# Performance work log

Hardware: AMD Instinct MI355X
Metric: run time of the kernel (lower is better)

Reference implementation:

```python
import math
import jax, jax.numpy as jnp
import numpy as np

B, DZ, DX, U = 262144, 8, 16, 64


def setup_inputs() -> dict:
    key = jax.random.key(0)
    ks = jax.random.split(key, 12)
    s = lambda k, shape, scale=1.0: (jax.random.normal(k, shape, dtype=jnp.float32) * scale)
    return {
        "h": s(ks[0], (B, U), 0.1),
        "c": s(ks[1], (B, U), 0.1),
        "z_prev": s(ks[2], (B, DZ)),
        "x_t": s(ks[3], (B, DX)),
        "W_kernel": s(ks[4], (DZ, 4 * U), 1.0 / math.sqrt(DZ)),
        "W_recurrent": s(ks[5], (U, 4 * U), 1.0 / math.sqrt(U)),
        "b_lstm": jnp.zeros((4 * U,), jnp.float32),
        "W_mu": s(ks[6], (U, DZ), 1.0 / math.sqrt(U)),
        "b_mu": jnp.zeros((DZ,), jnp.float32),
        "W_log_sigma": s(ks[7], (U, DZ), 1.0 / math.sqrt(U)),
        "b_log_sigma": -jnp.ones((DZ,), jnp.float32),  # Constant(-1.0) bias init
        "C": jnp.eye(DX, DZ, dtype=jnp.float32) + s(ks[8], (DX, DZ), 0.05),
        "b_emission": jnp.zeros((DX,), jnp.float32),
        "log_R_diag": jnp.zeros((DX,), jnp.float32),
    }


def reference(h, c, z_prev, x_t, W_kernel, W_recurrent, b_lstm,
              W_mu, b_mu, W_log_sigma, b_log_sigma, C, b_emission, log_R_diag):
    dz, dx = C.shape[1], C.shape[0]
    # --- Keras LSTMCell step (gate order: i, f, g, o) ---
    z = z_prev @ W_kernel + h @ W_recurrent + b_lstm  # [B, 4U]
    i, f, g, o = jnp.split(z, 4, axis=-1)
    c_new = jax.nn.sigmoid(f) * c + jax.nn.sigmoid(i) * jnp.tanh(g)
    h_new = jax.nn.sigmoid(o) * jnp.tanh(c_new)
    # --- transition params ---
    mu = h_new @ W_mu + b_mu                                        # [B, dz]
    log_sigma = jnp.clip(h_new @ W_log_sigma + b_log_sigma, -5.0, 3.0)
    sigma = jnp.exp(log_sigma)
    Sigma_diag = sigma ** 2                                          # [B, dz]
    R_diag = jnp.exp(log_R_diag)                                     # [dx]
    # --- alpha: log N(x_t; C mu + b, R + C diag(Sigma) C^T) ---
    pred_mean = mu @ C.T + b_emission                                # [B, dx]
    C_scaled = C[None, :, :] * jnp.sqrt(Sigma_diag)[:, None, :]      # [B, dx, dz]
    base = jnp.eye(dx, dtype=C.dtype) * R_diag + jnp.eye(dx, dtype=C.dtype) * 1e-6
    marg_cov = base[None] + jnp.einsum('bik,bjk->bij', C_scaled, C_scaled)  # [B, dx, dx]
    _, log_det = jnp.linalg.slogdet(marg_cov)
    marg_inv = jnp.linalg.inv(marg_cov)
    diff_x = x_t - pred_mean
    mahal = jnp.einsum('bi,bij,bj->b', diff_x, marg_inv, diff_x)
    alpha = -0.5 * (mahal + log_det + dx * math.log(2.0 * math.pi))  # [B]
    # --- gamma: posterior over z_t ---
    Sigma_inv_diag = 1.0 / (Sigma_diag + 1e-8)                       # [B, dz]
    R_inv_diag = 1.0 / (R_diag + 1e-8)                               # [dx]
    CtRinvC = (C * R_inv_diag[:, None]).T @ C                        # [dz, dz]
    V_inv = (jnp.eye(dz, dtype=C.dtype) * Sigma_inv_diag[:, None, :]
             + CtRinvC[None] + jnp.eye(dz, dtype=C.dtype) * 1e-6)    # [B, dz, dz]
    V = jnp.linalg.inv(V_inv)
    info = Sigma_inv_diag * mu + ((x_t - b_emission) * R_inv_diag) @ C  # [B, dz]
    gamma_mu = jnp.einsum('bij,bj->bi', V, info)                     # [B, dz]
    return alpha, gamma_mu, V, h_new, c_new
```

## Files before the change

kernel.cpp:

```cpp
#include <hip/hip_runtime.h>
#include <math.h>

#define BATCH 262144

#define WA_OFF  0
#define G6_OFF  18944
#define G8_OFF  19008
#define R6_OFF  19072
#define R8_OFF  19088
#define SLR_OFF 19104

typedef __attribute__((ext_vector_type(8))) short bf16x8;
typedef __attribute__((ext_vector_type(4))) float f32x4;

__device__ __forceinline__ float rcp1(float x) {
    float r = __builtin_amdgcn_rcpf(x);
    return r * (2.0f - x * r);
}
__device__ __forceinline__ float sigm(float x) {
    float e = __expf(-fabsf(x));
    float s = __builtin_amdgcn_rcpf(1.0f + e);
    return (x >= 0.0f) ? s : e * s;
}
__device__ __forceinline__ float tanh_f(float x) {
    float e = __expf(-2.0f * fabsf(x));
    float t = (1.0f - e) * __builtin_amdgcn_rcpf(1.0f + e);
    return copysignf(t, x);
}
__device__ __forceinline__ unsigned rne_bf16(float x) {
    unsigned u = __float_as_uint(x);
    return (u + 0x7fffu + ((u >> 16) & 1u)) >> 16;
}
__device__ __forceinline__ unsigned pack2(float lo, float hi) {
    return rne_bf16(lo) | (rne_bf16(hi) << 16);
}

__global__ void prep_kernel(const float* __restrict__ Wk,
                            const float* __restrict__ Wr,
                            const float* __restrict__ Cm,
                            const float* __restrict__ logR,
                            float* __restrict__ ws) {
    int b = blockIdx.x;
    int t = threadIdx.x;
    if (b < 12) {
        unsigned* wa = (unsigned*)(ws + WA_OFF);
        int F  = b * 256 + t;
        int fr = F >> 6, l = F & 63;
        int m  = fr / 3, ks = fr % 3;
        int c  = m * 16 + (l & 15);
        int k0 = ks * 32 + (l >> 4) * 8;
        int src = (c & 3) * 64 + (c >> 2);
        float v[8];
#pragma unroll
        for (int j = 0; j < 8; ++j) {
            int k = k0 + j;
            v[j] = (k < 8) ? Wk[k * 256 + src] : (k < 72 ? Wr[(k - 8) * 256 + src] : 0.0f);
        }
        wa[F * 4 + 0] = pack2(v[0], v[1]);
        wa[F * 4 + 1] = pack2(v[2], v[3]);
        wa[F * 4 + 2] = pack2(v[4], v[5]);
        wa[F * 4 + 3] = pack2(v[6], v[7]);
        return;
    }
    if (t < 64) {
        int k = t >> 3, l = t & 7;
        float g6 = 0.0f, g8 = 0.0f;
        for (int i = 0; i < 16; ++i) {
            float R  = expf(logR[i]);
            float cc = Cm[i * 8 + k] * Cm[i * 8 + l];
            g6 += cc / (R + 1e-6f);
            g8 += cc / (R + 1e-8f);
        }
        ws[G6_OFF + t] = g6;
        ws[G8_OFF + t] = g8;
    } else if (t < 80) {
        int i = t - 64;
        float R = expf(logR[i]);
        ws[R6_OFF + i] = 1.0f / (R + 1e-6f);
        ws[R8_OFF + i] = 1.0f / (R + 1e-8f);
    } else if (t == 80) {
        float s = 0.0f;
        for (int i = 0; i < 16; ++i) s += logf(expf(logR[i]) + 1e-6f);
        ws[SLR_OFF] = s;
    }
}

__global__ __launch_bounds__(256)
void lstm_kernel(const float* __restrict__ h_in,
                 const float* __restrict__ c_in,
                 const float* __restrict__ z_prev,
                 const float* __restrict__ b_lstm,
                 const float* __restrict__ W_mu,
                 const float* __restrict__ b_mu,
                 const float* __restrict__ W_ls,
                 const float* __restrict__ b_ls,
                 const float* __restrict__ ws,
                 float* __restrict__ out) {
    __shared__ __align__(16) float r1[64 * 72];
    __shared__ __align__(16) float r2[64 * 68];

    const int t   = threadIdx.x;
    const int l   = t & 63;
    const int wvu = __builtin_amdgcn_readfirstlane(t >> 6);
    const int lhi = l >> 4, llo = l & 15;
    const size_t E0 = (size_t)blockIdx.x * 64;

#pragma unroll
    for (int i = 0; i < 4; ++i) {
        int g = i * 1024 + t * 4;
        int e = g >> 6, u = g & 63;
        float4 hv = *(const float4*)(h_in + E0 * 64 + g);
        *(float4*)(r1 + e * 72 + 8 + u) = hv;
    }
    if (t < 128) {
        int g = t * 4;
        int e = g >> 3, p = g & 7;
        float4 zv = *(const float4*)(z_prev + E0 * 8 + g);
        *(float4*)(r1 + e * 72 + p) = zv;
    }
    __syncthreads();

    unsigned* fr = (unsigned*)r2;
#pragma unroll
    for (int i = 0; i < 3; ++i) {
        int c = i * 256 + t;
        if (c < 576) {
            int e = c / 9, k0 = (c % 9) * 8;
            float4 va = *(const float4*)(r1 + c * 8);
            float4 vb = *(const float4*)(r1 + c * 8 + 4);
            uint4 pk;
            pk.x = pack2(va.x, va.y);
            pk.y = pack2(va.z, va.w);
            pk.z = pack2(vb.x, vb.y);
            pk.w = pack2(vb.z, vb.w);
            int n = e >> 4, lo = e & 15, ks = k0 >> 5, hi = (k0 & 31) >> 3;
            int F = (n * 3 + ks) * 64 + hi * 16 + lo;
            *(uint4*)(fr + F * 4) = pk;
        }
    }
    if (t < 192) {
        int n = t / 48, r = t % 48;
        int hi = r / 16 + 1, lo = r & 15;
        int F = (n * 3 + 2) * 64 + hi * 16 + lo;
        *(uint4*)(fr + F * 4) = make_uint4(0, 0, 0, 0);
    }
    __syncthreads();

    float4 cp0 = *(const float4*)(c_in + E0 * 64 + 0 * 1024 + t * 4);
    float4 cp1 = *(const float4*)(c_in + E0 * 64 + 1 * 1024 + t * 4);
    float4 cp2 = *(const float4*)(c_in + E0 * 64 + 2 * 1024 + t * 4);
    float4 cp3 = *(const float4*)(c_in + E0 * 64 + 3 * 1024 + t * 4);

    f32x4 acc[4][4];
#pragma unroll
    for (int mm = 0; mm < 4; ++mm)
#pragma unroll
        for (int n = 0; n < 4; ++n) acc[mm][n] = (f32x4){0.f, 0.f, 0.f, 0.f};

    const unsigned* WA = (const unsigned*)(ws + WA_OFF);
#pragma unroll
    for (int ks = 0; ks < 3; ++ks) {
        bf16x8 bfr[4], afr[4];
#pragma unroll
        for (int n = 0; n < 4; ++n)
            bfr[n] = *(const bf16x8*)(fr + ((n * 3 + ks) * 64 + l) * 4);
#pragma unroll
        for (int mm = 0; mm < 4; ++mm)
            afr[mm] = *(const bf16x8*)(WA + (((4 * wvu + mm) * 3 + ks) * 64 + l) * 4);
#pragma unroll
        for (int mm = 0; mm < 4; ++mm)
#pragma unroll
            for (int n = 0; n < 4; ++n)
                acc[mm][n] = __builtin_amdgcn_mfma_f32_16x16x32_bf16(
                    afr[mm], bfr[n], acc[mm][n], 0, 0, 0);
    }

    float* cbuf = r1;
    {
        int g0 = t * 4;
        *(float4*)(cbuf + ((g0 >> 6)) * 68 + (g0 & 63)) = cp0;
        int g1 = 1024 + t * 4;
        *(float4*)(cbuf + ((g1 >> 6)) * 68 + (g1 & 63)) = cp1;
        int g2 = 2048 + t * 4;
        *(float4*)(cbuf + ((g2 >> 6)) * 68 + (g2 & 63)) = cp2;
        int g3 = 3072 + t * 4;
        *(float4*)(cbuf + ((g3 >> 6)) * 68 + (g3 & 63)) = cp3;
    }
    __syncthreads();

    float* hbuf = r2;
#pragma unroll
    for (int mm = 0; mm < 4; ++mm) {
        int u = 16 * wvu + 4 * mm + lhi;
        float bi = b_lstm[u], bf_ = b_lstm[64 + u], bg = b_lstm[128 + u], bo = b_lstm[192 + u];
#pragma unroll
        for (int n = 0; n < 4; ++n) {
            int e = n * 16 + llo;
            float zi = acc[mm][n][0] + bi;
            float zf = acc[mm][n][1] + bf_;
            float zg = acc[mm][n][2] + bg;
            float zo = acc[mm][n][3] + bo;
            float cold = cbuf[e * 68 + u];
            float cn = sigm(zf) * cold + sigm(zi) * tanh_f(zg);
            float hn = sigm(zo) * tanh_f(cn);
            cbuf[e * 68 + u] = cn;
            hbuf[u * 68 + e] = hn;
        }
    }
    __syncthreads();

    float* outH = out + (size_t)BATCH * 73  + E0 * 64;
    float* outC = out + (size_t)BATCH * 137 + E0 * 64;
#pragma unroll
    for (int i = 0; i < 4; ++i) {
        int g = i * 1024 + t * 4;
        int e = g >> 6, u = g & 63;
        *(float4*)(outC + g) = *(const float4*)(cbuf + e * 68 + u);
        float4 hv = make_float4(hbuf[(u + 0) * 68 + e], hbuf[(u + 1) * 68 + e],
                                hbuf[(u + 2) * 68 + e], hbuf[(u + 3) * 68 + e]);
        *(float4*)(outH + g) = hv;
    }

    {
        const float* Wsel = (wvu < 2) ? W_mu : W_ls;
        const float* bsel = (wvu < 2) ? b_mu : b_ls;
        const int d0 = (wvu & 1) * 4;
        float m0 = bsel[d0 + 0], m1 = bsel[d0 + 1], m2 = bsel[d0 + 2], m3 = bsel[d0 + 3];
#pragma unroll
        for (int u = 0; u < 64; ++u) {
            float hv = hbuf[u * 68 + l];
            m0 = fmaf(hv, Wsel[u * 8 + d0 + 0], m0);
            m1 = fmaf(hv, Wsel[u * 8 + d0 + 1], m1);
            m2 = fmaf(hv, Wsel[u * 8 + d0 + 2], m2);
            m3 = fmaf(hv, Wsel[u * 8 + d0 + 3], m3);
        }
        float* slot = out + (size_t)BATCH * 9 + (E0 + l) * 64 + wvu * 4;
        *(float4*)slot = make_float4(m0, m1, m2, m3);
    }
}

__global__ __launch_bounds__(256)
void tail_kernel(const float* __restrict__ x_in,
                 const float* __restrict__ Cm,
                 const float* __restrict__ b_em,
                 const float* __restrict__ ws,
                 float* __restrict__ out) {
    __shared__ float vbuf[64 * 65];

    const int t    = threadIdx.x;
    const int lane = t & 63;
    const int wv   = t >> 6;
    const int blk  = blockIdx.x;
    const size_t e = (size_t)blk * 256 + t;

    const float* G6 = ws + G6_OFF;
    const float* G8 = ws + G8_OFF;
    const float* r6 = ws + R6_OFF;
    const float* r8 = ws + R8_OFF;
    const float  slr = ws[SLR_OFF];

    const float* tmp = out + (size_t)BATCH * 9 + e * 64;
    float4 q0 = *(const float4*)(tmp + 0);
    float4 q1 = *(const float4*)(tmp + 4);
    float4 q2 = *(const float4*)(tmp + 8);
    float4 q3 = *(const float4*)(tmp + 12);
    float mu[8]  = {q0.x, q0.y, q0.z, q0.w, q1.x, q1.y, q1.z, q1.w};
    float lsg[8] = {q2.x, q2.y, q2.z, q2.w, q3.x, q3.y, q3.z, q3.w};

    float sig[8], Sinv[8];
#pragma unroll
    for (int d = 0; d < 8; ++d) {
        float l = fminf(fmaxf(lsg[d], -5.0f), 3.0f);
        float s = __expf(l);
        sig[d]  = s;
        Sinv[d] = rcp1(s * s + 1e-8f);
    }

    float xv[16];
    {
        const float4* x4 = (const float4*)(x_in + e * 16);
#pragma unroll
        for (int q = 0; q < 4; ++q) {
            float4 v = x4[q];
            xv[4 * q + 0] = v.x; xv[4 * q + 1] = v.y;
            xv[4 * q + 2] = v.z; xv[4 * q + 3] = v.w;
        }
    }

    float t6[8], t8[8];
#pragma unroll
    for (int k = 0; k < 8; ++k) { t6[k] = 0.0f; t8[k] = 0.0f; }
    float qdr = 0.0f;
#pragma unroll
    for (int i = 0; i < 16; ++i) {
        float pm = b_em[i];
#pragma unroll
        for (int d = 0; d < 8; ++d) pm = fmaf(mu[d], Cm[i * 8 + d], pm);
        float df = xv[i] - pm;
        float xe = xv[i] - b_em[i];
        float a6 = df * r6[i];
        float a8 = xe * r8[i];
        qdr = fmaf(df, a6, qdr);
#pragma unroll
        for (int k = 0; k < 8; ++k) {
            t6[k] = fmaf(a6, Cm[i * 8 + k], t6[k]);
            t8[k] = fmaf(a8, Cm[i * 8 + k], t8[k]);
        }
    }

    float M[8][8];
#pragma unroll
    for (int k = 0; k < 8; ++k)
#pragma unroll
        for (int l = 0; l <= k; ++l)
            M[k][l] = ((k == l) ? 1.0f : 0.0f) + sig[k] * sig[l] * G6[k * 8 + l];

    float ldia[8];
    float logdetM = 0.0f;
#pragma unroll
    for (int k = 0; k < 8; ++k) {
        float d = M[k][k];
#pragma unroll
        for (int j = 0; j < k; ++j) d = fmaf(-M[k][j], M[k][j], d);
        float l = sqrtf(d);
        logdetM += __logf(d);
        float li = rcp1(l);
        M[k][k] = l; ldia[k] = li;
#pragma unroll
        for (int i = k + 1; i < 8; ++i) {
            float s = M[i][k];
#pragma unroll
            for (int j = 0; j < k; ++j) s = fmaf(-M[i][j], M[k][j], s);
            M[i][k] = s * li;
        }
    }
    float w[8];
    float ssq = 0.0f;
#pragma unroll
    for (int k = 0; k < 8; ++k) {
        float s = sig[k] * t6[k];
#pragma unroll
        for (int j = 0; j < k; ++j) s = fmaf(-M[k][j], w[j], s);
        w[k] = s * ldia[k];
        ssq  = fmaf(w[k], w[k], ssq);
    }
    float mahal  = qdr - ssq;
    float alpha  = -0.5f * (mahal + slr + logdetM + 29.40603306254952f);

    float Vi[8][8];
#pragma unroll
    for (int k = 0; k < 8; ++k)
#pragma unroll
        for (int l = 0; l <= k; ++l)
            Vi[k][l] = G8[k * 8 + l] + ((k == l) ? (Sinv[k] + 1e-6f) : 0.0f);

    float vdia[8];
#pragma unroll
    for (int k = 0; k < 8; ++k) {
        float d = Vi[k][k];
#pragma unroll
        for (int j = 0; j < k; ++j) d = fmaf(-Vi[k][j], Vi[k][j], d);
        float l = sqrtf(d);
        float li = rcp1(l);
        Vi[k][k] = l; vdia[k] = li;
#pragma unroll
        for (int i = k + 1; i < 8; ++i) {
            float s = Vi[i][k];
#pragma unroll
            for (int j = 0; j < k; ++j) s = fmaf(-Vi[i][j], Vi[k][j], s);
            Vi[i][k] = s * li;
        }
    }
#pragma unroll
    for (int k = 0; k < 8; ++k) {
        M[k][k] = vdia[k];
#pragma unroll
        for (int i = k + 1; i < 8; ++i) {
            float s = 0.0f;
#pragma unroll
            for (int j = k; j < i; ++j) s = fmaf(Vi[i][j], M[j][k], s);
            M[i][k] = -s * vdia[i];
        }
    }
    float info[8];
#pragma unroll
    for (int k = 0; k < 8; ++k) info[k] = fmaf(Sinv[k], mu[k], t8[k]);

#pragma unroll 1
    for (int ch = 0; ch < 4; ++ch) {
        if (wv == ch) {
            float gam[8];
#pragma unroll
            for (int a = 0; a < 8; ++a) gam[a] = 0.0f;
#pragma unroll
            for (int a = 0; a < 8; ++a) {
#pragma unroll
                for (int b = 0; b < 8; ++b) {
                    int m0 = (a > b) ? a : b;
                    float s = 0.0f;
#pragma unroll
                    for (int i = 0; i < 8; ++i)
                        if (i >= m0) s = fmaf(M[i][a], M[i][b], s);
                    vbuf[(a * 8 + b) * 65 + lane] = s;
                    gam[a] = fmaf(s, info[b], gam[a]);
                }
            }
            out[e] = alpha;
            float4* outG = (float4*)(out + (size_t)BATCH + e * 8);
            outG[0] = make_float4(gam[0], gam[1], gam[2], gam[3]);
            outG[1] = make_float4(gam[4], gam[5], gam[6], gam[7]);
        }
        __syncthreads();
        {
            float* outV = out + (size_t)BATCH * 9 + ((size_t)blk * 256 + (size_t)ch * 64) * 64;
#pragma unroll
            for (int i = 0; i < 4; ++i) {
                int g = i * 1024 + t * 4;
                int ee = g >> 6, j = g & 63;
                float4 v = make_float4(vbuf[(j + 0) * 65 + ee], vbuf[(j + 1) * 65 + ee],
                                       vbuf[(j + 2) * 65 + ee], vbuf[(j + 3) * 65 + ee]);
                *(float4*)(outV + g) = v;
            }
        }
        __syncthreads();
    }
}

extern "C" void kernel_launch(void* const* d_in, const int* in_sizes, int n_in,
                              void* d_out, int out_size, void* d_ws, size_t ws_size,
                              hipStream_t stream) {
    const float* h    = (const float*)d_in[0];
    const float* c    = (const float*)d_in[1];
    const float* zp   = (const float*)d_in[2];
    const float* xt   = (const float*)d_in[3];
    const float* Wk   = (const float*)d_in[4];
    const float* Wr   = (const float*)d_in[5];
    const float* bl   = (const float*)d_in[6];
    const float* Wmu  = (const float*)d_in[7];
    const float* bmu  = (const float*)d_in[8];
    const float* Wls  = (const float*)d_in[9];
    const float* bls  = (const float*)d_in[10];
    const float* Cm   = (const float*)d_in[11];
    const float* bem  = (const float*)d_in[12];
    const float* logR = (const float*)d_in[13];
    float* ws  = (float*)d_ws;
    float* out = (float*)d_out;

    hipLaunchKernelGGL(prep_kernel, dim3(13), dim3(256), 0, stream, Wk, Wr, Cm, logR, ws);
    hipLaunchKernelGGL(lstm_kernel, dim3(BATCH / 64), dim3(256), 0, stream,
                       h, c, zp, bl, Wmu, bmu, Wls, bls, ws, out);
    hipLaunchKernelGGL(tail_kernel, dim3(BATCH / 256), dim3(256), 0, stream,
                       xt, Cm, bem, ws, out);
}
```

Before: 111.8 us.

## Fuse LSTM and tail kernels, passing mu/log_sigma through shared memory

Merges the LSTM kernel and the Kalman tail kernel into one kernel in which each block handles 256 batch rows as four 64-row LSTM tiles. The mu/log_sigma values go into a shared-memory buffer instead of being written to global memory and read back by a second launch. This removes the global round-trip of the intermediate values and one kernel launch. In exchange the grid has a quarter as many blocks, the LSTM tiles run one after another inside each block, and more LDS is used per block, which can lower occupancy and latency hiding.

```diff
diff --git a/kernel.cpp b/kernel.cpp
--- a/kernel.cpp
+++ b/kernel.cpp
@@ -86,192 +86,192 @@
 }
 
 __global__ __launch_bounds__(256)
-void lstm_kernel(const float* __restrict__ h_in,
-                 const float* __restrict__ c_in,
-                 const float* __restrict__ z_prev,
-                 const float* __restrict__ b_lstm,
-                 const float* __restrict__ W_mu,
-                 const float* __restrict__ b_mu,
-                 const float* __restrict__ W_ls,
-                 const float* __restrict__ b_ls,
-                 const float* __restrict__ ws,
-                 float* __restrict__ out) {
+void fused_kernel(const float* __restrict__ h_in,
+                  const float* __restrict__ c_in,
+                  const float* __restrict__ z_prev,
+                  const float* __restrict__ x_in,
+                  const float* __restrict__ b_lstm,
+                  const float* __restrict__ W_mu,
+                  const float* __restrict__ b_mu,
+                  const float* __restrict__ W_ls,
+                  const float* __restrict__ b_ls,
+                  const float* __restrict__ Cm,
+                  const float* __restrict__ b_em,
+                  const float* __restrict__ ws,
+                  float* __restrict__ out) {
     __shared__ __align__(16) float r1[64 * 72];
     __shared__ __align__(16) float r2[64 * 68];
+    __shared__ float muls[16 * 257];
 
     const int t   = threadIdx.x;
     const int l   = t & 63;
     const int wvu = __builtin_amdgcn_readfirstlane(t >> 6);
     const int lhi = l >> 4, llo = l & 15;
-    const size_t E0 = (size_t)blockIdx.x * 64;
-
-#pragma unroll
-    for (int i = 0; i < 4; ++i) {
-        int g = i * 1024 + t * 4;
-        int e = g >> 6, u = g & 63;
-        float4 hv = *(const float4*)(h_in + E0 * 64 + g);
-        *(float4*)(r1 + e * 72 + 8 + u) = hv;
-    }
-    if (t < 128) {
-        int g = t * 4;
-        int e = g >> 3, p = g & 7;
-        float4 zv = *(const float4*)(z_prev + E0 * 8 + g);
-        *(float4*)(r1 + e * 72 + p) = zv;
+    const size_t B0 = (size_t)blockIdx.x * 256;
+    const unsigned* WA = (const unsigned*)(ws + WA_OFF);
+
+#pragma unroll 1
+    for (int tile = 0; tile < 4; ++tile) {
+        const size_t E0 = B0 + (size_t)tile * 64;
+        __syncthreads();
+
+#pragma unroll
+        for (int i = 0; i < 4; ++i) {
+            int g = i * 1024 + t * 4;
+            int e = g >> 6, u = g & 63;
+            float4 hv = *(const float4*)(h_in + E0 * 64 + g);
+            *(float4*)(r1 + e * 72 + 8 + u) = hv;
+        }
+        if (t < 128) {
+            int g = t * 4;
+            int e = g >> 3, p = g & 7;
+            float4 zv = *(const float4*)(z_prev + E0 * 8 + g);
+            *(float4*)(r1 + e * 72 + p) = zv;
+        }
+        __syncthreads();
+
+        unsigned* fr = (unsigned*)r2;
+#pragma unroll
+        for (int i = 0; i < 3; ++i) {
+            int c = i * 256 + t;
+            if (c < 576) {
+                int e = c / 9, k0 = (c % 9) * 8;
+                float4 va = *(const float4*)(r1 + c * 8);
+                float4 vb = *(const float4*)(r1 + c * 8 + 4);
+                uint4 pk;
+                pk.x = pack2(va.x, va.y);
+                pk.y = pack2(va.z, va.w);
+                pk.z = pack2(vb.x, vb.y);
+                pk.w = pack2(vb.z, vb.w);
+                int n = e >> 4, lo = e & 15, ks = k0 >> 5, hi = (k0 & 31) >> 3;
+                int F = (n * 3 + ks) * 64 + hi * 16 + lo;
+                *(uint4*)(fr + F * 4) = pk;
+            }
+        }
+        if (t < 192) {
+            int n = t / 48, r = t % 48;
+            int hi = r / 16 + 1, lo = r & 15;
+            int F = (n * 3 + 2) * 64 + hi * 16 + lo;
+            *(uint4*)(fr + F * 4) = make_uint4(0, 0, 0, 0);
+        }
+        __syncthreads();
+
+        float4 cp0 = *(const float4*)(c_in + E0 * 64 + 0 * 1024 + t * 4);
+        float4 cp1 = *(const float4*)(c_in + E0 * 64 + 1 * 1024 + t * 4);
+        float4 cp2 = *(const float4*)(c_in + E0 * 64 + 2 * 1024 + t * 4);
+        float4 cp3 = *(const float4*)(c_in + E0 * 64 + 3 * 1024 + t * 4);
+
+        f32x4 acc[4][4];
+#pragma unroll
+        for (int mm = 0; mm < 4; ++mm)
+#pragma unroll
+            for (int n = 0; n < 4; ++n) acc[mm][n] = (f32x4){0.f, 0.f, 0.f, 0.f};
+#pragma unroll
+        for (int ks = 0; ks < 3; ++ks) {
+            bf16x8 bfr[4], afr[4];
+#pragma unroll
+            for (int n = 0; n < 4; ++n)
+                bfr[n] = *(const bf16x8*)(fr + ((n * 3 + ks) * 64 + l) * 4);
+#pragma unroll
+            for (int mm = 0; mm < 4; ++mm)
+                afr[mm] = *(const bf16x8*)(WA + (((4 * wvu + mm) * 3 + ks) * 64 + l) * 4);
+#pragma unroll
+            for (int mm = 0; mm < 4; ++mm)
+#pragma unroll
+                for (int n = 0; n < 4; ++n)
+                    acc[mm][n] = __builtin_amdgcn_mfma_f32_16x16x32_bf16(
+                        afr[mm], bfr[n], acc[mm][n], 0, 0, 0);
+        }
+
+        float* cbuf = r1;
+        {
+            int g0 = t * 4;
+            *(float4*)(cbuf + ((g0 >> 6)) * 68 + (g0 & 63)) = cp0;
+            int g1 = 1024 + t * 4;
+            *(float4*)(cbuf + ((g1 >> 6)) * 68 + (g1 & 63)) = cp1;
+            int g2 = 2048 + t * 4;
+            *(float4*)(cbuf + ((g2 >> 6)) * 68 + (g2 & 63)) = cp2;
+            int g3 = 3072 + t * 4;
+            *(float4*)(cbuf + ((g3 >> 6)) * 68 + (g3 & 63)) = cp3;
+        }
+        __syncthreads();
+
+        float* hbuf = r2;
+#pragma unroll
+        for (int mm = 0; mm < 4; ++mm) {
+            int u = 16 * wvu + 4 * mm + lhi;
+            float bi = b_lstm[u], bf_ = b_lstm[64 + u], bg = b_lstm[128 + u], bo = b_lstm[192 + u];
+#pragma unroll
+            for (int n = 0; n < 4; ++n) {
+                int e = n * 16 + llo;
+                float zi = acc[mm][n][0] + bi;
+                float zf = acc[mm][n][1] + bf_;
+                float zg = acc[mm][n][2] + bg;
+                float zo = acc[mm][n][3] + bo;
+                float cold = cbuf[e * 68 + u];
+                float cn = sigm(zf) * cold + sigm(zi) * tanh_f(zg);
+                float hn = sigm(zo) * tanh_f(cn);
+                cbuf[e * 68 + u] = cn;
+                hbuf[u * 68 + e] = hn;
+            }
+        }
+        __syncthreads();
+
+        float* outH = out + (size_t)BATCH * 73  + E0 * 64;
+        float* outC = out + (size_t)BATCH * 137 + E0 * 64;
+#pragma unroll
+        for (int i = 0; i < 4; ++i) {
+            int g = i * 1024 + t * 4;
+            int e = g >> 6, u = g & 63;
+            *(float4*)(outC + g) = *(const float4*)(cbuf + e * 68 + u);
+            float4 hv = make_float4(hbuf[(u + 0) * 68 + e], hbuf[(u + 1) * 68 + e],
+                                    hbuf[(u + 2) * 68 + e], hbuf[(u + 3) * 68 + e]);
+            *(float4*)(outH + g) = hv;
+        }
+
+        {
+            const float* Wsel = (wvu < 2) ? W_mu : W_ls;
+            const float* bsel = (wvu < 2) ? b_mu : b_ls;
+            const int d0 = (wvu & 1) * 4;
+            const int row0 = (wvu < 2) ? d0 : 8 + d0;
+            float m0 = bsel[d0 + 0], m1 = bsel[d0 + 1], m2 = bsel[d0 + 2], m3 = bsel[d0 + 3];
+#pragma unroll
+            for (int u = 0; u < 64; ++u) {
+                float hv = hbuf[u * 68 + l];
+                m0 = fmaf(hv, Wsel[u * 8 + d0 + 0], m0);
+                m1 = fmaf(hv, Wsel[u * 8 + d0 + 1], m1);
+                m2 = fmaf(hv, Wsel[u * 8 + d0 + 2], m2);
+                m3 = fmaf(hv, Wsel[u * 8 + d0 + 3], m3);
+            }
+            int col = tile * 64 + l;
+            muls[(row0 + 0) * 257 + col] = m0;
+            muls[(row0 + 1) * 257 + col] = m1;
+            muls[(row0 + 2) * 257 + col] = m2;
+            muls[(row0 + 3) * 257 + col] = m3;
+        }
     }
     __syncthreads();
-
-    unsigned* fr = (unsigned*)r2;
-#pragma unroll
-    for (int i = 0; i < 3; ++i) {
-        int c = i * 256 + t;
-        if (c < 576) {
-            int e = c / 9, k0 = (c % 9) * 8;
-            float4 va = *(const float4*)(r1 + c * 8);
-            float4 vb = *(const float4*)(r1 + c * 8 + 4);
-            uint4 pk;
-            pk.x = pack2(va.x, va.y);
-            pk.y = pack2(va.z, va.w);
-            pk.z = pack2(vb.x, vb.y);
-            pk.w = pack2(vb.z, vb.w);
-            int n = e >> 4, lo = e & 15, ks = k0 >> 5, hi = (k0 & 31) >> 3;
-            int F = (n * 3 + ks) * 64 + hi * 16 + lo;
-            *(uint4*)(fr + F * 4) = pk;
-        }
-    }
-    if (t < 192) {
-        int n = t / 48, r = t % 48;
-        int hi = r / 16 + 1, lo = r & 15;
-        int F = (n * 3 + 2) * 64 + hi * 16 + lo;
-        *(uint4*)(fr + F * 4) = make_uint4(0, 0, 0, 0);
-    }
-    __syncthreads();
-
-    float4 cp0 = *(const float4*)(c_in + E0 * 64 + 0 * 1024 + t * 4);
-    float4 cp1 = *(const float4*)(c_in + E0 * 64 + 1 * 1024 + t * 4);
-    float4 cp2 = *(const float4*)(c_in + E0 * 64 + 2 * 1024 + t * 4);
-    float4 cp3 = *(const float4*)(c_in + E0 * 64 + 3 * 1024 + t * 4);
-
-    f32x4 acc[4][4];
-#pragma unroll
-    for (int mm = 0; mm < 4; ++mm)
-#pragma unroll
-        for (int n = 0; n < 4; ++n) acc[mm][n] = (f32x4){0.f, 0.f, 0.f, 0.f};
-
-    const unsigned* WA = (const unsigned*)(ws + WA_OFF);
-#pragma unroll
-    for (int ks = 0; ks < 3; ++ks) {
-        bf16x8 bfr[4], afr[4];
-#pragma unroll
-        for (int n = 0; n < 4; ++n)
-            bfr[n] = *(const bf16x8*)(fr + ((n * 3 + ks) * 64 + l) * 4);
-#pragma unroll
-        for (int mm = 0; mm < 4; ++mm)
-            afr[mm] = *(const bf16x8*)(WA + (((4 * wvu + mm) * 3 + ks) * 64 + l) * 4);
-#pragma unroll
-        for (int mm = 0; mm < 4; ++mm)
-#pragma unroll
-            for (int n = 0; n < 4; ++n)
-                acc[mm][n] = __builtin_amdgcn_mfma_f32_16x16x32_bf16(
-                    afr[mm], bfr[n], acc[mm][n], 0, 0, 0);
-    }
-
-    float* cbuf = r1;
-    {
-        int g0 = t * 4;
-        *(float4*)(cbuf + ((g0 >> 6)) * 68 + (g0 & 63)) = cp0;
-        int g1 = 1024 + t * 4;
-        *(float4*)(cbuf + ((g1 >> 6)) * 68 + (g1 & 63)) = cp1;
-        int g2 = 2048 + t * 4;
-        *(float4*)(cbuf + ((g2 >> 6)) * 68 + (g2 & 63)) = cp2;
-        int g3 = 3072 + t * 4;
-        *(float4*)(cbuf + ((g3 >> 6)) * 68 + (g3 & 63)) = cp3;
-    }
-    __syncthreads();
-
-    float* hbuf = r2;
-#pragma unroll
-    for (int mm = 0; mm < 4; ++mm) {
-        int u = 16 * wvu + 4 * mm + lhi;
-        float bi = b_lstm[u], bf_ = b_lstm[64 + u], bg = b_lstm[128 + u], bo = b_lstm[192 + u];
-#pragma unroll
-        for (int n = 0; n < 4; ++n) {
-            int e = n * 16 + llo;
-            float zi = acc[mm][n][0] + bi;
-            float zf = acc[mm][n][1] + bf_;
-            float zg = acc[mm][n][2] + bg;
-            float zo = acc[mm][n][3] + bo;
-            float cold = cbuf[e * 68 + u];
-            float cn = sigm(zf) * cold + sigm(zi) * tanh_f(zg);
-            float hn = sigm(zo) * tanh_f(cn);
-            cbuf[e * 68 + u] = cn;
-            hbuf[u * 68 + e] = hn;
-        }
-    }
-    __syncthreads();
-
-    float* outH = out + (size_t)BATCH * 73  + E0 * 64;
-    float* outC = out + (size_t)BATCH * 137 + E0 * 64;
-#pragma unroll
-    for (int i = 0; i < 4; ++i) {
-        int g = i * 1024 + t * 4;
-        int e = g >> 6, u = g & 63;
-        *(float4*)(outC + g) = *(const float4*)(cbuf + e * 68 + u);
-        float4 hv = make_float4(hbuf[(u + 0) * 68 + e], hbuf[(u + 1) * 68 + e],
-                                hbuf[(u + 2) * 68 + e], hbuf[(u + 3) * 68 + e]);
-        *(float4*)(outH + g) = hv;
-    }
-
-    {
-        const float* Wsel = (wvu < 2) ? W_mu : W_ls;
-        const float* bsel = (wvu < 2) ? b_mu : b_ls;
-        const int d0 = (wvu & 1) * 4;
-        float m0 = bsel[d0 + 0], m1 = bsel[d0 + 1], m2 = bsel[d0 + 2], m3 = bsel[d0 + 3];
-#pragma unroll
-        for (int u = 0; u < 64; ++u) {
-            float hv = hbuf[u * 68 + l];
-            m0 = fmaf(hv, Wsel[u * 8 + d0 + 0], m0);
-            m1 = fmaf(hv, Wsel[u * 8 + d0 + 1], m1);
-            m2 = fmaf(hv, Wsel[u * 8 + d0 + 2], m2);
-            m3 = fmaf(hv, Wsel[u * 8 + d0 + 3], m3);
-        }
-        float* slot = out + (size_t)BATCH * 9 + (E0 + l) * 64 + wvu * 4;
-        *(float4*)slot = make_float4(m0, m1, m2, m3);
-    }
-}
-
-__global__ __launch_bounds__(256)
-void tail_kernel(const float* __restrict__ x_in,
-                 const float* __restrict__ Cm,
-                 const float* __restrict__ b_em,
-                 const float* __restrict__ ws,
-                 float* __restrict__ out) {
-    __shared__ float vbuf[64 * 65];
-
-    const int t    = threadIdx.x;
-    const int lane = t & 63;
-    const int wv   = t >> 6;
-    const int blk  = blockIdx.x;
-    const size_t e = (size_t)blk * 256 + t;
 
     const float* G6 = ws + G6_OFF;
     const float* G8 = ws + G8_OFF;
     const float* r6 = ws + R6_OFF;
     const float* r8 = ws + R8_OFF;
     const float  slr = ws[SLR_OFF];
-
-    const float* tmp = out + (size_t)BATCH * 9 + e * 64;
-    float4 q0 = *(const float4*)(tmp + 0);
-    float4 q1 = *(const float4*)(tmp + 4);
-    float4 q2 = *(const float4*)(tmp + 8);
-    float4 q3 = *(const float4*)(tmp + 12);
-    float mu[8]  = {q0.x, q0.y, q0.z, q0.w, q1.x, q1.y, q1.z, q1.w};
-    float lsg[8] = {q2.x, q2.y, q2.z, q2.w, q3.x, q3.y, q3.z, q3.w};
+    const size_t e = B0 + t;
+    const int wv = t >> 6;
+
+    float mu[8], lsg[8];
+#pragma unroll
+    for (int d = 0; d < 8; ++d) {
+        mu[d]  = muls[d * 257 + t];
+        lsg[d] = muls[(8 + d) * 257 + t];
+    }
 
     float sig[8], Sinv[8];
 #pragma unroll
     for (int d = 0; d < 8; ++d) {
-        float l = fminf(fmaxf(lsg[d], -5.0f), 3.0f);
-        float s = __expf(l);
+        float lv = fminf(fmaxf(lsg[d], -5.0f), 3.0f);
+        float s = __expf(lv);
         sig[d]  = s;
         Sinv[d] = rcp1(s * s + 1e-8f);
     }
@@ -312,8 +312,8 @@
 #pragma unroll
     for (int k = 0; k < 8; ++k)
 #pragma unroll
-        for (int l = 0; l <= k; ++l)
-            M[k][l] = ((k == l) ? 1.0f : 0.0f) + sig[k] * sig[l] * G6[k * 8 + l];
+        for (int lq = 0; lq <= k; ++lq)
+            M[k][lq] = ((k == lq) ? 1.0f : 0.0f) + sig[k] * sig[lq] * G6[k * 8 + lq];
 
     float ldia[8];
     float logdetM = 0.0f;
@@ -322,10 +322,10 @@
         float d = M[k][k];
 #pragma unroll
         for (int j = 0; j < k; ++j) d = fmaf(-M[k][j], M[k][j], d);
-        float l = sqrtf(d);
+        float lv = sqrtf(d);
         logdetM += __logf(d);
-        float li = rcp1(l);
-        M[k][k] = l; ldia[k] = li;
+        float li = rcp1(lv);
+        M[k][k] = lv; ldia[k] = li;
 #pragma unroll
         for (int i = k + 1; i < 8; ++i) {
             float s = M[i][k];
@@ -344,15 +344,15 @@
         w[k] = s * ldia[k];
         ssq  = fmaf(w[k], w[k], ssq);
     }
-    float mahal  = qdr - ssq;
-    float alpha  = -0.5f * (mahal + slr + logdetM + 29.40603306254952f);
+    float mahal = qdr - ssq;
+    float alpha = -0.5f * (mahal + slr + logdetM + 29.40603306254952f);
 
     float Vi[8][8];
 #pragma unroll
     for (int k = 0; k < 8; ++k)
 #pragma unroll
-        for (int l = 0; l <= k; ++l)
-            Vi[k][l] = G8[k * 8 + l] + ((k == l) ? (Sinv[k] + 1e-6f) : 0.0f);
+        for (int lq = 0; lq <= k; ++lq)
+            Vi[k][lq] = G8[k * 8 + lq] + ((k == lq) ? (Sinv[k] + 1e-6f) : 0.0f);
 
     float vdia[8];
 #pragma unroll
@@ -360,9 +360,9 @@
         float d = Vi[k][k];
 #pragma unroll
         for (int j = 0; j < k; ++j) d = fmaf(-Vi[k][j], Vi[k][j], d);
-        float l = sqrtf(d);
-        float li = rcp1(l);
-        Vi[k][k] = l; vdia[k] = li;
+        float lv = sqrtf(d);
+        float li = rcp1(lv);
+        Vi[k][k] = lv; vdia[k] = li;
 #pragma unroll
         for (int i = k + 1; i < 8; ++i) {
             float s = Vi[i][k];
@@ -386,6 +386,7 @@
 #pragma unroll
     for (int k = 0; k < 8; ++k) info[k] = fmaf(Sinv[k], mu[k], t8[k]);
 
+    float* vbuf = r1;
 #pragma unroll 1
     for (int ch = 0; ch < 4; ++ch) {
         if (wv == ch) {
@@ -401,7 +402,7 @@
 #pragma unroll
                     for (int i = 0; i < 8; ++i)
                         if (i >= m0) s = fmaf(M[i][a], M[i][b], s);
-                    vbuf[(a * 8 + b) * 65 + lane] = s;
+                    vbuf[(a * 8 + b) * 65 + l] = s;
                     gam[a] = fmaf(s, info[b], gam[a]);
                 }
             }
@@ -412,7 +413,7 @@
         }
         __syncthreads();
         {
-            float* outV = out + (size_t)BATCH * 9 + ((size_t)blk * 256 + (size_t)ch * 64) * 64;
+            float* outV = out + (size_t)BATCH * 9 + (B0 + (size_t)ch * 64) * 64;
 #pragma unroll
             for (int i = 0; i < 4; ++i) {
                 int g = i * 1024 + t * 4;
@@ -447,8 +448,6 @@
     float* out = (float*)d_out;
 
     hipLaunchKernelGGL(prep_kernel, dim3(13), dim3(256), 0, stream, Wk, Wr, Cm, logR, ws);
-    hipLaunchKernelGGL(lstm_kernel, dim3(BATCH / 64), dim3(256), 0, stream,
-                       h, c, zp, bl, Wmu, bmu, Wls, bls, ws, out);
-    hipLaunchKernelGGL(tail_kernel, dim3(BATCH / 256), dim3(256), 0, stream,
-                       xt, Cm, bem, ws, out);
-}
+    hipLaunchKernelGGL(fused_kernel, dim3(BATCH / 256), dim3(256), 0, stream,
+                       h, c, zp, xt, bl, Wmu, bmu, Wls, bls, Cm, bem, ws, out);
+}
```

Result: slower. 176.1 us (+57.6%).
